# Performance work log

Measured on AMD Instinct MI355X. Metric: run time of the kernel, lower is better.

The kernel has to match this reference:

```python
import jax, jax.numpy as jnp
import numpy as np

B, S, E, A = 4, 2048, 1024, 1024

def setup_inputs() -> dict:
    key = jax.random.key(0)
    ks = jax.random.split(key, 6)
    scale = 1.0 / np.sqrt(E)
    return {
        "query": jax.random.normal(ks[0], (B, S, E), jnp.float32),
        "key": jax.random.normal(ks[1], (B, S, E), jnp.float32),
        "value": jax.random.normal(ks[2], (B, S, E), jnp.float32),
        "Wq": jax.random.normal(ks[3], (E, A), jnp.float32) * scale,
        "bq": jnp.zeros((A,), jnp.float32),
        "Wk": jax.random.normal(ks[4], (E, A), jnp.float32) * scale,
        "bk": jnp.zeros((A,), jnp.float32),
        "Wv": jax.random.normal(ks[5], (E, A), jnp.float32) * scale,
        "bv": jnp.zeros((A,), jnp.float32),
    }

def reference(query, key, value, Wq, bq, Wk, bk, Wv, bv):
    # QKV linear projections: [B,S,E] @ [E,A] + [A]
    q = jnp.einsum("bse,ea->bsa", query, Wq) + bq
    k = jnp.einsum("bse,ea->bsa", key, Wk) + bk
    v = jnp.einsum("bse,ea->bsa", value, Wv) + bv
    # scaled dot-product attention (no mask, single head)
    inv_sqrt_d = 1.0 / jnp.sqrt(jnp.asarray(A, q.dtype))
    scores = jnp.einsum("bqa,bka->bqk", q, k) * inv_sqrt_d  # [B,S,S]
    probs = jax.nn.softmax(scores, axis=-1)
    return jnp.einsum("bqk,bka->bqa", probs, v)
```

## Files before the change

### kernel.cpp

```cpp
#include <hip/hip_runtime.h>

typedef unsigned short u16;
typedef __attribute__((ext_vector_type(16))) float f32x16;
typedef __attribute__((ext_vector_type(8))) short s16x8;
typedef __attribute__((ext_vector_type(8))) unsigned short u16x8;
typedef __attribute__((ext_vector_type(4))) unsigned short u16x4;

__device__ __forceinline__ u16 f2b(float x) {
  union { float f; unsigned u; } v; v.f = x;
  unsigned r = v.u + 0x7fffu + ((v.u >> 16) & 1u);
  return (u16)(r >> 16);
}
__device__ __forceinline__ float b2f(u16 x) {
  union { unsigned u; float f; } v; v.u = ((unsigned)x) << 16;
  return v.f;
}

__global__ __launch_bounds__(256) void cast3_f32_bf16(const float* __restrict__ s0,
                                                      const float* __restrict__ s1,
                                                      const float* __restrict__ s2,
                                                      u16* __restrict__ dst, long n4) {
  const float* src = (blockIdx.y == 0) ? s0 : ((blockIdx.y == 1) ? s1 : s2);
  long i = blockIdx.x * 256 + threadIdx.x;
  if (i >= n4) return;
  float4 f = ((const float4*)src)[i];
  u16x4 o;
  o.x = f2b(f.x); o.y = f2b(f.y); o.z = f2b(f.z); o.w = f2b(f.w);
  ((u16x4*)(dst + blockIdx.y * n4 * 4))[i] = o;
}

__global__ __launch_bounds__(256) void transpose_cast_w3(const float* __restrict__ w0,
                                                         const float* __restrict__ w1,
                                                         const float* __restrict__ w2,
                                                         u16* __restrict__ Wt, int E_, int A_) {
  __shared__ float tile[32][33];
  const float* W = (blockIdx.z == 0) ? w0 : ((blockIdx.z == 1) ? w1 : w2);
  u16* dst = Wt + (long)blockIdx.z * E_ * A_;
  int a0 = blockIdx.x * 32, e0 = blockIdx.y * 32;
  int tx = threadIdx.x & 31, ty = threadIdx.x >> 5;
  for (int i = ty; i < 32; i += 8) tile[i][tx] = W[(long)(e0 + i) * A_ + a0 + tx];
  __syncthreads();
  for (int i = ty; i < 32; i += 8) dst[(long)(a0 + i) * E_ + e0 + tx] = f2b(tile[tx][i]);
}

template<bool OUT_BF16>
__global__ __launch_bounds__(256)
void gemm_bt(const u16* __restrict__ Ag, const u16* __restrict__ Bg,
             const float* __restrict__ b0, const float* __restrict__ b1,
             const float* __restrict__ b2, void* __restrict__ Cg,
             int M, int N, int K, float scale, long sA, long sB, long sC,
             int XM, int XN, u16* __restrict__ VtG, long vtB, int vtS) {
  __shared__ u16 As[128 * 32];
  __shared__ u16 Bs[128 * 32];
  const int t = threadIdx.x;
  const int wave = t >> 6, lane = t & 63;
  const int l32 = lane & 31, hi = lane >> 5;
  const int wm = wave & 1, wn = wave >> 1;

  const int gn = gridDim.x, gm = gridDim.y;
  const int L = blockIdx.y * gn + blockIdx.x;
  const int c = L & 7, tt = L >> 3;
  const int sm = gm / XM, sn = gn / XN;
  const int cm = c % XM, cn = c / XM;
  const int tm = tt % sm, tn = tt / sm;
  const int m0 = (cm * sm + tm) * 128;
  const int n0 = (cn * sn + tn) * 128;

  const int z = blockIdx.z;
  const float* bias = (z == 0) ? b0 : ((z == 1) ? b1 : b2);
  const long zA = (long)z * sA;
  const long zB = (long)z * sB;
  const long zC = (long)z * sC;

  const int ar = t >> 2, ac = (t & 3) * 8;
  const u16* Ap0 = Ag + zA + (long)(m0 + ar) * K + ac;
  const u16* Ap1 = Ag + zA + (long)(m0 + 64 + ar) * K + ac;
  const u16* Bp0 = Bg + zB + (long)(n0 + ar) * K + ac;
  const u16* Bp1 = Bg + zB + (long)(n0 + 64 + ar) * K + ac;
  u16* AsD0 = As + wave * 512;
  u16* AsD1 = As + 2048 + wave * 512;
  u16* BsD0 = Bs + wave * 512;
  u16* BsD1 = Bs + 2048 + wave * 512;

  f32x16 acc[2][2] = {};

  const u16* Ard = As + (wm * 64 + l32) * 32 + hi * 8;
  const u16* Brd = Bs + (wn * 64 + l32) * 32 + hi * 8;

  for (int k0 = 0; k0 < K; k0 += 32) {
    __builtin_amdgcn_global_load_lds(
        (const __attribute__((address_space(1))) unsigned int*)(Ap0 + k0),
        (__attribute__((address_space(3))) unsigned int*)AsD0, 16, 0, 0);
    __builtin_amdgcn_global_load_lds(
        (const __attribute__((address_space(1))) unsigned int*)(Ap1 + k0),
        (__attribute__((address_space(3))) unsigned int*)AsD1, 16, 0, 0);
    __builtin_amdgcn_global_load_lds(
        (const __attribute__((address_space(1))) unsigned int*)(Bp0 + k0),
        (__attribute__((address_space(3))) unsigned int*)BsD0, 16, 0, 0);
    __builtin_amdgcn_global_load_lds(
        (const __attribute__((address_space(1))) unsigned int*)(Bp1 + k0),
        (__attribute__((address_space(3))) unsigned int*)BsD1, 16, 0, 0);
    __syncthreads();

    s16x8 fa[2][2], fb[2][2];
#pragma unroll
    for (int i = 0; i < 2; i++)
#pragma unroll
      for (int kk = 0; kk < 2; kk++) {
        fa[i][kk] = *(const s16x8*)(Ard + i * 1024 + kk * 16);
        fb[i][kk] = *(const s16x8*)(Brd + i * 1024 + kk * 16);
      }
#pragma unroll
    for (int kk = 0; kk < 2; kk++)
#pragma unroll
      for (int i = 0; i < 2; i++)
#pragma unroll
        for (int j = 0; j < 2; j++)
          acc[i][j] = __builtin_amdgcn_mfma_f32_32x32x16_bf16(fa[i][kk], fb[j][kk],
                                                              acc[i][j], 0, 0, 0);
    __syncthreads();
  }

  float bj[2];
#pragma unroll
  for (int j = 0; j < 2; j++) {
    int col = n0 + wn * 64 + j * 32 + l32;
    bj[j] = bias ? bias[col] : 0.0f;
  }

  if (OUT_BF16 && VtG != nullptr && z == 2) {
    const int b = m0 / vtS;
    const int smod = m0 % vtS;
    u16* vbase = VtG + (long)b * vtB + smod;
#pragma unroll
    for (int i = 0; i < 2; i++)
#pragma unroll
      for (int j = 0; j < 2; j++) {
        int col = n0 + wn * 64 + j * 32 + l32;
        u16* cb = vbase + (long)col * vtS + wm * 64 + i * 32 + 4 * hi;
#pragma unroll
        for (int g = 0; g < 4; g++) {
          u16x4 o;
#pragma unroll
          for (int rr = 0; rr < 4; rr++) o[rr] = f2b(acc[i][j][g * 4 + rr] * scale + bj[j]);
          *(u16x4*)(cb + g * 8) = o;
        }
      }
  } else {
#pragma unroll
    for (int i = 0; i < 2; i++)
#pragma unroll
      for (int j = 0; j < 2; j++) {
        int col = n0 + wn * 64 + j * 32 + l32;
#pragma unroll
        for (int r = 0; r < 16; r++) {
          long row = m0 + wm * 64 + i * 32 + (r & 3) + 8 * (r >> 2) + 4 * hi;
          float v = acc[i][j][r] * scale + bj[j];
          long ro = zC + row * (long)N + col;
          if (OUT_BF16) ((u16*)Cg)[ro] = f2b(v);
          else          ((float*)Cg)[ro] = v;
        }
      }
  }
}

__device__ __forceinline__ float wred_max(float x) {
  for (int o = 32; o > 0; o >>= 1) x = fmaxf(x, __shfl_xor(x, o));
  return x;
}
__device__ __forceinline__ float wred_sum(float x) {
  for (int o = 32; o > 0; o >>= 1) x += __shfl_xor(x, o);
  return x;
}

__global__ __launch_bounds__(256) void softmax_rows_bf16(const u16* __restrict__ S,
                                                         u16* __restrict__ P, int ncols) {
  long row = blockIdx.x;
  const u16x8* s8 = (const u16x8*)(S + row * (long)ncols);
  int t = threadIdx.x;
  int wave = t >> 6, lane = t & 63;
  u16x8 a = s8[t];
  float f[8];
#pragma unroll
  for (int i = 0; i < 8; i++) f[i] = b2f(a[i]);
  float m = f[0];
#pragma unroll
  for (int i = 1; i < 8; i++) m = fmaxf(m, f[i]);
  m = wred_max(m);
  __shared__ float redm[4], reds[4];
  if (lane == 0) redm[wave] = m;
  __syncthreads();
  m = fmaxf(fmaxf(redm[0], redm[1]), fmaxf(redm[2], redm[3]));

  float e[8], s = 0.f;
#pragma unroll
  for (int i = 0; i < 8; i++) { e[i] = __expf(f[i] - m); s += e[i]; }
  s = wred_sum(s);
  if (lane == 0) reds[wave] = s;
  __syncthreads();
  s = reds[0] + reds[1] + reds[2] + reds[3];
  float inv = 1.0f / s;

  u16x8 o;
#pragma unroll
  for (int i = 0; i < 8; i++) o[i] = f2b(e[i] * inv);
  ((u16x8*)(P + row * (long)ncols))[t] = o;
}

extern "C" void kernel_launch(void* const* d_in, const int* in_sizes, int n_in,
                              void* d_out, int out_size, void* d_ws, size_t ws_size,
                              hipStream_t stream) {
  const float* query = (const float*)d_in[0];
  const float* key_  = (const float*)d_in[1];
  const float* value = (const float*)d_in[2];
  const float* Wq = (const float*)d_in[3];
  const float* bq = (const float*)d_in[4];
  const float* Wk = (const float*)d_in[5];
  const float* bk = (const float*)d_in[6];
  const float* Wv = (const float*)d_in[7];
  const float* bv = (const float*)d_in[8];

  constexpr int B = 4, S = 2048, E = 1024, A = 1024;
  constexpr long MB = 1024 * 1024;
  char* ws = (char*)d_ws;
  u16* Qb  = (u16*)(ws + 0 * MB);
  u16* Kb  = (u16*)(ws + 16 * MB);
  u16* Vt  = (u16*)(ws + 48 * MB);
  u16* P   = (u16*)(ws + 64 * MB);
  u16* Sc  = (u16*)(ws + 96 * MB);
  u16* Xq  = (u16*)(ws + 96 * MB);
  u16* WqT = (u16*)(ws + 144 * MB);

  const long n = (long)B * S * E;
  const long n4 = n / 4;
  dim3 blk(256);

  cast3_f32_bf16<<<dim3(n4 / 256, 3), blk, 0, stream>>>(query, key_, value, Xq, n4);

  transpose_cast_w3<<<dim3(A / 32, E / 32, 3), blk, 0, stream>>>(Wq, Wk, Wv, WqT, E, A);

  dim3 pg(A / 128, (B * S) / 128, 3);
  gemm_bt<true><<<pg, blk, 0, stream>>>(Xq, WqT, bq, bk, bv, Qb,
                                        B * S, A, E, 1.0f,
                                        (long)8 * MB, (long)1 * MB, (long)8 * MB,
                                        8, 1, Vt, (long)A * S, S);

  dim3 sg(S / 128, S / 128, B);
  gemm_bt<true><<<sg, blk, 0, stream>>>(Qb, Kb, nullptr, nullptr, nullptr, Sc,
                                        S, S, A, 0.03125f,
                                        (long)S * A, (long)S * A, (long)S * S,
                                        4, 2, nullptr, 0, 0);

  softmax_rows_bf16<<<dim3(B * S), blk, 0, stream>>>(Sc, P, S);

  dim3 og(A / 128, S / 128, B);
  gemm_bt<false><<<og, blk, 0, stream>>>(P, Vt, nullptr, nullptr, nullptr, (float*)d_out,
                                         S, A, S, 1.0f,
                                         (long)S * S, (long)S * A, (long)S * A,
                                         4, 2, nullptr, 0, 0);
}
```

Measured before the change: 360.5 us.

## Widen GEMM block tile to 128x256 and add occupancy launch bound

```diff
diff --git a/kernel.cpp b/kernel.cpp
--- a/kernel.cpp
+++ b/kernel.cpp
@@ -44,14 +44,14 @@
 }
 
 template<bool OUT_BF16>
-__global__ __launch_bounds__(256)
+__global__ __launch_bounds__(256, 2)
 void gemm_bt(const u16* __restrict__ Ag, const u16* __restrict__ Bg,
              const float* __restrict__ b0, const float* __restrict__ b1,
              const float* __restrict__ b2, void* __restrict__ Cg,
              int M, int N, int K, float scale, long sA, long sB, long sC,
              int XM, int XN, u16* __restrict__ VtG, long vtB, int vtS) {
   __shared__ u16 As[128 * 32];
-  __shared__ u16 Bs[128 * 32];
+  __shared__ u16 Bs[256 * 32];
   const int t = threadIdx.x;
   const int wave = t >> 6, lane = t & 63;
   const int l32 = lane & 31, hi = lane >> 5;
@@ -64,7 +64,7 @@
   const int cm = c % XM, cn = c / XM;
   const int tm = tt % sm, tn = tt / sm;
   const int m0 = (cm * sm + tm) * 128;
-  const int n0 = (cn * sn + tn) * 128;
+  const int n0 = (cn * sn + tn) * 256;
 
   const int z = blockIdx.z;
   const float* bias = (z == 0) ? b0 : ((z == 1) ? b1 : b2);
@@ -72,59 +72,60 @@
   const long zB = (long)z * sB;
   const long zC = (long)z * sC;
 
-  const int ar = t >> 2, ac = (t & 3) * 8;
-  const u16* Ap0 = Ag + zA + (long)(m0 + ar) * K + ac;
-  const u16* Ap1 = Ag + zA + (long)(m0 + 64 + ar) * K + ac;
-  const u16* Bp0 = Bg + zB + (long)(n0 + ar) * K + ac;
-  const u16* Bp1 = Bg + zB + (long)(n0 + 64 + ar) * K + ac;
-  u16* AsD0 = As + wave * 512;
-  u16* AsD1 = As + 2048 + wave * 512;
-  u16* BsD0 = Bs + wave * 512;
-  u16* BsD1 = Bs + 2048 + wave * 512;
-
-  f32x16 acc[2][2] = {};
+  const int lr = lane >> 2, lc = (lane & 3) * 8;
+  const u16* Ap0 = Ag + zA + (long)(m0 + (wave)      * 16 + lr) * K + lc;
+  const u16* Ap1 = Ag + zA + (long)(m0 + (wave + 4)  * 16 + lr) * K + lc;
+  const u16* Bp0 = Bg + zB + (long)(n0 + (wave)      * 16 + lr) * K + lc;
+  const u16* Bp1 = Bg + zB + (long)(n0 + (wave + 4)  * 16 + lr) * K + lc;
+  const u16* Bp2 = Bg + zB + (long)(n0 + (wave + 8)  * 16 + lr) * K + lc;
+  const u16* Bp3 = Bg + zB + (long)(n0 + (wave + 12) * 16 + lr) * K + lc;
+  u16* AsD0 = As + (wave)      * 512;
+  u16* AsD1 = As + (wave + 4)  * 512;
+  u16* BsD0 = Bs + (wave)      * 512;
+  u16* BsD1 = Bs + (wave + 4)  * 512;
+  u16* BsD2 = Bs + (wave + 8)  * 512;
+  u16* BsD3 = Bs + (wave + 12) * 512;
+
+  f32x16 acc[2][4] = {};
 
   const u16* Ard = As + (wm * 64 + l32) * 32 + hi * 8;
-  const u16* Brd = Bs + (wn * 64 + l32) * 32 + hi * 8;
+  const u16* Brd = Bs + (wn * 128 + l32) * 32 + hi * 8;
 
   for (int k0 = 0; k0 < K; k0 += 32) {
-    __builtin_amdgcn_global_load_lds(
-        (const __attribute__((address_space(1))) unsigned int*)(Ap0 + k0),
-        (__attribute__((address_space(3))) unsigned int*)AsD0, 16, 0, 0);
-    __builtin_amdgcn_global_load_lds(
-        (const __attribute__((address_space(1))) unsigned int*)(Ap1 + k0),
-        (__attribute__((address_space(3))) unsigned int*)AsD1, 16, 0, 0);
-    __builtin_amdgcn_global_load_lds(
-        (const __attribute__((address_space(1))) unsigned int*)(Bp0 + k0),
-        (__attribute__((address_space(3))) unsigned int*)BsD0, 16, 0, 0);
-    __builtin_amdgcn_global_load_lds(
-        (const __attribute__((address_space(1))) unsigned int*)(Bp1 + k0),
-        (__attribute__((address_space(3))) unsigned int*)BsD1, 16, 0, 0);
+#define GLD(src, dst) __builtin_amdgcn_global_load_lds( \
+        (const __attribute__((address_space(1))) unsigned int*)(src + k0), \
+        (__attribute__((address_space(3))) unsigned int*)(dst), 16, 0, 0)
+    GLD(Ap0, AsD0); GLD(Ap1, AsD1);
+    GLD(Bp0, BsD0); GLD(Bp1, BsD1); GLD(Bp2, BsD2); GLD(Bp3, BsD3);
+#undef GLD
     __syncthreads();
 
-    s16x8 fa[2][2], fb[2][2];
+    s16x8 fa[2][2], fb[4][2];
 #pragma unroll
     for (int i = 0; i < 2; i++)
 #pragma unroll
-      for (int kk = 0; kk < 2; kk++) {
+      for (int kk = 0; kk < 2; kk++)
         fa[i][kk] = *(const s16x8*)(Ard + i * 1024 + kk * 16);
-        fb[i][kk] = *(const s16x8*)(Brd + i * 1024 + kk * 16);
-      }
+#pragma unroll
+    for (int j = 0; j < 4; j++)
+#pragma unroll
+      for (int kk = 0; kk < 2; kk++)
+        fb[j][kk] = *(const s16x8*)(Brd + j * 1024 + kk * 16);
 #pragma unroll
     for (int kk = 0; kk < 2; kk++)
 #pragma unroll
       for (int i = 0; i < 2; i++)
 #pragma unroll
-        for (int j = 0; j < 2; j++)
+        for (int j = 0; j < 4; j++)
           acc[i][j] = __builtin_amdgcn_mfma_f32_32x32x16_bf16(fa[i][kk], fb[j][kk],
                                                               acc[i][j], 0, 0, 0);
     __syncthreads();
   }
 
-  float bj[2];
-#pragma unroll
-  for (int j = 0; j < 2; j++) {
-    int col = n0 + wn * 64 + j * 32 + l32;
+  float bj[4];
+#pragma unroll
+  for (int j = 0; j < 4; j++) {
+    int col = n0 + wn * 128 + j * 32 + l32;
     bj[j] = bias ? bias[col] : 0.0f;
   }
 
@@ -135,8 +136,8 @@
 #pragma unroll
     for (int i = 0; i < 2; i++)
 #pragma unroll
-      for (int j = 0; j < 2; j++) {
-        int col = n0 + wn * 64 + j * 32 + l32;
+      for (int j = 0; j < 4; j++) {
+        int col = n0 + wn * 128 + j * 32 + l32;
         u16* cb = vbase + (long)col * vtS + wm * 64 + i * 32 + 4 * hi;
 #pragma unroll
         for (int g = 0; g < 4; g++) {
@@ -150,8 +151,8 @@
 #pragma unroll
     for (int i = 0; i < 2; i++)
 #pragma unroll
-      for (int j = 0; j < 2; j++) {
-        int col = n0 + wn * 64 + j * 32 + l32;
+      for (int j = 0; j < 4; j++) {
+        int col = n0 + wn * 128 + j * 32 + l32;
 #pragma unroll
         for (int r = 0; r < 16; r++) {
           long row = m0 + wm * 64 + i * 32 + (r & 3) + 8 * (r >> 2) + 4 * hi;
@@ -239,13 +240,13 @@
 
   transpose_cast_w3<<<dim3(A / 32, E / 32, 3), blk, 0, stream>>>(Wq, Wk, Wv, WqT, E, A);
 
-  dim3 pg(A / 128, (B * S) / 128, 3);
+  dim3 pg(A / 256, (B * S) / 128, 3);
   gemm_bt<true><<<pg, blk, 0, stream>>>(Xq, WqT, bq, bk, bv, Qb,
                                         B * S, A, E, 1.0f,
                                         (long)8 * MB, (long)1 * MB, (long)8 * MB,
                                         8, 1, Vt, (long)A * S, S);
 
-  dim3 sg(S / 128, S / 128, B);
+  dim3 sg(S / 256, S / 128, B);
   gemm_bt<true><<<sg, blk, 0, stream>>>(Qb, Kb, nullptr, nullptr, nullptr, Sc,
                                         S, S, A, 0.03125f,
                                         (long)S * A, (long)S * A, (long)S * S,
@@ -253,7 +254,7 @@
 
   softmax_rows_bf16<<<dim3(B * S), blk, 0, stream>>>(Sc, P, S);
 
-  dim3 og(A / 128, S / 128, B);
+  dim3 og(A / 256, S / 128, B);
   gemm_bt<false><<<og, blk, 0, stream>>>(P, Vt, nullptr, nullptr, nullptr, (float*)d_out,
                                          S, A, S, 1.0f,
                                          (long)S * S, (long)S * A, (long)S * A,
```

Result: slower. 373.0 us (+3.5%).
